# Performance work log

Hardware: AMD Instinct MI355X
Metric: run time of the kernel (lower is better)

Reference implementation:

```python
import jax, jax.numpy as jnp
import numpy as np

NUM_FEATURES = 256   # 2**8
BOND_DIM = 16
N_CORES = 8          # log2(NUM_FEATURES)
BATCH = 262144


def _mpo_cores(mpo_weights, n, bond_dim):
    # Slice the flat parameter vector into n cores of shape (l, r, 2, 2).
    shapes = [(1, bond_dim, 2, 2)] + [(bond_dim, bond_dim, 2, 2)] * (n - 2) + [(bond_dim, 1, 2, 2)]
    cores, off = [], 0
    for s in shapes:
        sz = int(np.prod(s))
        cores.append(mpo_weights[off:off + sz].reshape(s))
        off += sz
    return cores


def _contract_mpo(cores):
    # Sequentially contract the tensor-train cores into the full (2^n, 2^n) matrix.
    # T has axes (bond, I, J) where I/J accumulate the row/col physical bits
    # in order i1..in / j1..jn, matching the original einsum + reshape.
    T = cores[0][0]          # (r, 2, 2)
    dim = 2
    for A in cores[1:]:      # A: (l, r2, 2, 2)
        T = jnp.einsum('aIJ,abkm->bIkJm', T, A).reshape(A.shape[1], dim * 2, dim * 2)
        dim *= 2
    return T[0]              # (2^n, 2^n)


def setup_inputs() -> dict:
    key = jax.random.key(0)
    k1, k2, k3 = jax.random.split(key, 3)
    total = 2 * 4 * BOND_DIM + (N_CORES - 2) * 4 * BOND_DIM ** 2  # 6272
    return {
        'x': jax.random.normal(k1, (BATCH, NUM_FEATURES), dtype=jnp.float32),
        'mpo_weights': jax.random.normal(k2, (total,), dtype=jnp.float32) * 0.1,
        'dense_kernel': jax.random.normal(k3, (NUM_FEATURES, 1), dtype=jnp.float32) * 0.1,
        'dense_bias': jnp.zeros((1,), dtype=jnp.float32),
    }


def reference(x, mpo_weights, dense_kernel, dense_bias):
    W = _contract_mpo(_mpo_cores(mpo_weights, N_CORES, BOND_DIM))  # (256, 256)
    h = jnp.square(x @ W)                                          # (B, 256)
    return h @ dense_kernel + dense_bias                           # (B, 1)
```

## Files before the change

### kernel.cpp

```cpp
#include <hip/hip_runtime.h>
#include <hip/hip_bf16.h>

typedef _Float16 half8 __attribute__((ext_vector_type(8)));
typedef float    floatx4 __attribute__((ext_vector_type(4)));

#define WSCALE      4096.0f
#define WSCALE_INV  (1.0f/(4096.0f*4096.0f))

#define T1_OFF   0
#define U_OFF    4096
#define WF16_OFF 8192

__global__ __launch_bounds__(256)
void mpo_prep1(const float* __restrict__ w, float* __restrict__ ws) {
    __shared__ __align__(16) float wL[3136];
    __shared__ __align__(16) float sL[4352];
    const int tid = threadIdx.x;

    {
        const floatx4* s4 = reinterpret_cast<const floatx4*>(w + blockIdx.x * 3136);
        floatx4* d4 = reinterpret_cast<floatx4*>(wL);
        for (int i = tid; i < 784; i += 256) d4[i] = s4[i];
    }
    __syncthreads();

    if (blockIdx.x == 0) {
        {
            int li = tid;
            int mm = li & 3, kk = (li >> 2) & 3, c = li >> 4;
            int k1 = kk >> 1, k2 = kk & 1, m1 = mm >> 1, m2 = mm & 1;
            float s = 0.f;
#pragma unroll
            for (int b = 0; b < 16; ++b)
                s += wL[b * 4 + k1 * 2 + m1] * wL[64 + b * 64 + c * 4 + k2 * 2 + m2];
            sL[li] = s;
        }
        {
            const int i0 = (tid >> 4) * 4, j0 = (tid & 15) * 4;
            const float* Ab = wL + 1088 + (i0 >> 2) * 64;
            const float* Bb = wL + 2112 + j0;
            float acc[4][4] = {};
#pragma unroll
            for (int b = 0; b < 16; ++b) {
                floatx4 ar = *reinterpret_cast<const floatx4*>(Ab + b * 4);
                floatx4 br = *reinterpret_cast<const floatx4*>(Bb + b * 64);
#pragma unroll
                for (int r = 0; r < 4; ++r)
#pragma unroll
                    for (int s = 0; s < 4; ++s) acc[r][s] += ar[r] * br[s];
            }
#pragma unroll
            for (int r = 0; r < 4; ++r)
#pragma unroll
            for (int s = 0; s < 4; ++s) {
                int i = i0 + r, j = j0 + s;
                sL[256 + (i >> 2) * 256 + (j >> 2) * 16 +
                   ((i >> 1) & 1) * 8 + ((j >> 1) & 1) * 4 + (i & 1) * 2 + (j & 1)] = acc[r][s];
            }
        }
        __syncthreads();
        {
            const int p0 = (tid >> 6) * 4, q0 = (tid & 63) * 4;
            float acc[4][4] = {};
#pragma unroll
            for (int a = 0; a < 16; ++a) {
                floatx4 pr = *reinterpret_cast<const floatx4*>(sL + a * 16 + p0);
                floatx4 qr = *reinterpret_cast<const floatx4*>(sL + 256 + a * 256 + q0);
#pragma unroll
                for (int r = 0; r < 4; ++r)
#pragma unroll
                    for (int s = 0; s < 4; ++s) acc[r][s] += pr[r] * qr[s];
            }
#pragma unroll
            for (int r = 0; r < 4; ++r)
#pragma unroll
            for (int s = 0; s < 4; ++s) {
                int p = p0 + r, q = q0 + s;
                ws[T1_OFF + (q >> 4) * 256 + ((p >> 2) * 4 + ((q >> 2) & 3)) * 16 +
                   (p & 3) * 4 + (q & 3)] = acc[r][s];
            }
        }
    } else {
        {
            const int i0 = (tid >> 4) * 4, j0 = (tid & 15) * 4;
            const float* Ab = wL + (i0 >> 2) * 64;
            const float* Bb = wL + 1024 + j0;
            float acc[4][4] = {};
#pragma unroll
            for (int b = 0; b < 16; ++b) {
                floatx4 ar = *reinterpret_cast<const floatx4*>(Ab + b * 4);
                floatx4 br = *reinterpret_cast<const floatx4*>(Bb + b * 64);
#pragma unroll
                for (int r = 0; r < 4; ++r)
#pragma unroll
                    for (int s = 0; s < 4; ++s) acc[r][s] += ar[r] * br[s];
            }
#pragma unroll
            for (int r = 0; r < 4; ++r)
#pragma unroll
            for (int s = 0; s < 4; ++s) {
                int i = i0 + r, j = j0 + s;
                sL[(i >> 2) * 256 + (j >> 2) * 16 +
                   ((i >> 1) & 1) * 8 + ((j >> 1) & 1) * 4 + (i & 1) * 2 + (j & 1)] = acc[r][s];
            }
        }
        {
            int li = tid;
            int mm = li & 3, kk = (li >> 2) & 3, a = li >> 4;
            int k1 = kk >> 1, k2 = kk & 1, m1 = mm >> 1, m2 = mm & 1;
            float s = 0.f;
#pragma unroll
            for (int b = 0; b < 16; ++b)
                s += wL[2048 + a * 64 + b * 4 + k1 * 2 + m1] * wL[3072 + b * 4 + k2 * 2 + m2];
            sL[4096 + li] = s;
        }
        __syncthreads();
        {
            const int r0 = (tid >> 2) * 4, q0 = (tid & 3) * 4;
            float acc[4][4] = {};
#pragma unroll
            for (int b = 0; b < 16; ++b) {
                floatx4 ar = *reinterpret_cast<const floatx4*>(sL + (r0 >> 4) * 256 + b * 16 + (r0 & 15));
                floatx4 br = *reinterpret_cast<const floatx4*>(sL + 4096 + b * 16 + q0);
#pragma unroll
                for (int r = 0; r < 4; ++r)
#pragma unroll
                    for (int s = 0; s < 4; ++s) acc[r][s] += ar[r] * br[s];
            }
#pragma unroll
            for (int r = 0; r < 4; ++r)
#pragma unroll
            for (int s = 0; s < 4; ++s)
                ws[U_OFF + (r0 + r) * 16 + q0 + s] = acc[r][s];
        }
    }
}

__global__ __launch_bounds__(256)
void mpo_prep2(const float* __restrict__ ws, _Float16* __restrict__ Wf) {
    int idx = blockIdx.x * blockDim.x + threadIdx.x;
    int J4 = idx & 255, I4 = idx >> 8;
    int I16 = I4 >> 4, kc = (I4 >> 2) & 3, k2 = I4 & 3;
    int J16 = J4 >> 4, mc = (J4 >> 2) & 3, m2 = J4 & 3;
    const float* T1 = ws + T1_OFF;
    const float* U  = ws + U_OFF + (((kc * 4 + mc) * 4 + k2) * 4 + m2);
    float s = 0.f;
#pragma unroll
    for (int a = 0; a < 16; ++a)
        s += T1[(a * 16 + I16) * 16 + J16] * U[a * 256];
    int n = J4 >> 4, lr = J4 & 15, kk = I4 >> 5, gg = (I4 >> 3) & 3, j = I4 & 7;
    Wf[(((n * 8 + kk) * 64) + gg * 16 + lr) * 8 + j] = (_Float16)(s * WSCALE);
}

__global__ __launch_bounds__(512, 2)
void mpo_main(const float* __restrict__ x, const _Float16* __restrict__ Wf,
              const float* __restrict__ dk, const float* __restrict__ bias,
              float* __restrict__ out) {
    extern __shared__ _Float16 Wl[];
    float* dkL = reinterpret_cast<float*>(Wl + 65536);

    const int tid  = threadIdx.x;
    const int lane = tid & 63;
    const int wave = tid >> 6;
    const int lrow = lane & 15;
    const int g    = lane >> 4;

    const long blockbase = (long)blockIdx.x * 1024;
    const float* xb0 = x + (blockbase + wave * 16 + lrow) * 256 + g * 8;

    half8 a[8];
    floatx4 loE[8], hiE[8], loO[8], hiO[8];

#define SB()  __builtin_amdgcn_sched_barrier(0)
#define NTL(p) __builtin_nontemporal_load(reinterpret_cast<const floatx4*>(p))
#define XLDE(i, xn) do { const float* p_ = (xn) + (i) * 32; loE[i] = NTL(p_); hiE[i] = NTL(p_ + 4); } while (0)
#define XLDO(i, xn) do { const float* p_ = (xn) + (i) * 32; loO[i] = NTL(p_); hiO[i] = NTL(p_ + 4); } while (0)
#define XLDE_ALL(xn) do { XLDE(0,xn); XLDE(1,xn); XLDE(2,xn); XLDE(3,xn); \
                          XLDE(4,xn); XLDE(5,xn); XLDE(6,xn); XLDE(7,xn); } while (0)
#define XLDO_ALL(xn) do { XLDO(0,xn); XLDO(1,xn); XLDO(2,xn); XLDO(3,xn); \
                          XLDO(4,xn); XLDO(5,xn); XLDO(6,xn); XLDO(7,xn); } while (0)
#define XCVTE(i) do { half8 f_;                                                \
                     f_[0] = (_Float16)loE[i][0]; f_[1] = (_Float16)loE[i][1]; \
                     f_[2] = (_Float16)loE[i][2]; f_[3] = (_Float16)loE[i][3]; \
                     f_[4] = (_Float16)hiE[i][0]; f_[5] = (_Float16)hiE[i][1]; \
                     f_[6] = (_Float16)hiE[i][2]; f_[7] = (_Float16)hiE[i][3]; \
                     a[i] = f_; } while (0)
#define XCVTO(i) do { half8 f_;                                                \
                     f_[0] = (_Float16)loO[i][0]; f_[1] = (_Float16)loO[i][1]; \
                     f_[2] = (_Float16)loO[i][2]; f_[3] = (_Float16)loO[i][3]; \
                     f_[4] = (_Float16)hiO[i][0]; f_[5] = (_Float16)hiO[i][1]; \
                     f_[6] = (_Float16)hiO[i][2]; f_[7] = (_Float16)hiO[i][3]; \
                     a[i] = f_; } while (0)
#define XCVTE_ALL() do { XCVTE(0); XCVTE(1); XCVTE(2); XCVTE(3); \
                         XCVTE(4); XCVTE(5); XCVTE(6); XCVTE(7); } while (0)
#define XCVTO_ALL() do { XCVTO(0); XCVTO(1); XCVTO(2); XCVTO(3); \
                         XCVTO(4); XCVTO(5); XCVTO(6); XCVTO(7); } while (0)

#define NLOOP(rp) do {                                                           \
    _Pragma("unroll 1")                                                          \
    for (int n = 0; n < 16; ++n) {                                               \
        const float kv = dkL[n * 16 + lrow];                                     \
        const half8* Wn = Wv + n * 512 + lane;                                   \
        floatx4 c0 = {0, 0, 0, 0};                                               \
        _Pragma("unroll")                                                        \
        for (int kk = 0; kk < 8; ++kk)                                           \
            c0 = __builtin_amdgcn_mfma_f32_16x16x32_f16(a[kk], Wn[kk * 64], c0, 0, 0, 0); \
        _Pragma("unroll")                                                        \
        for (int r = 0; r < 4; ++r) rp[r] += c0[r] * c0[r] * kv;                 \
    } } while (0)

#define REDUCE_STORE(rp, p) do {                                                 \
    _Pragma("unroll")                                                            \
    for (int r = 0; r < 4; ++r) {                                                \
        float v = rp[r];                                                         \
        v += __shfl_xor(v, 1); v += __shfl_xor(v, 2);                            \
        v += __shfl_xor(v, 4); v += __shfl_xor(v, 8);                            \
        rp[r] = v;                                                               \
    }                                                                            \
    if (lrow == 0) {                                                             \
        floatx4 o;                                                               \
        _Pragma("unroll")                                                        \
        for (int r = 0; r < 4; ++r) o[r] = rp[r] * WSCALE_INV + bs;              \
        *reinterpret_cast<floatx4*>(out + blockbase + (p) * 128 + wave * 16 + g * 4) = o; \
    } } while (0)

    XLDE_ALL(xb0);
    SB();
    {
        const floatx4* src = reinterpret_cast<const floatx4*>(Wf);
        floatx4* dst = reinterpret_cast<floatx4*>(Wl);
#pragma unroll
        for (int i = 0; i < 16; ++i)
            dst[tid + i * 512] = src[tid + i * 512];
    }
    if (tid < 256) dkL[tid] = dk[tid];
    const float bs = bias[0];
    __syncthreads();
    XLDO_ALL(xb0 + 128 * 256);
    SB();
    XCVTE_ALL();
    SB();

    const half8* Wv = reinterpret_cast<const half8*>(Wl);

#pragma unroll 1
    for (int pp = 0; pp < 8; pp += 2) {
        {
            float rp[4] = {0, 0, 0, 0};
            NLOOP(rp);
            if (pp + 2 < 8) { XLDE_ALL(xb0 + (pp + 2) * (128 * 256)); }
            SB();
            REDUCE_STORE(rp, pp);
            XCVTO_ALL();
            SB();
        }
        {
            float rp[4] = {0, 0, 0, 0};
            NLOOP(rp);
            if (pp + 3 < 8) { XLDO_ALL(xb0 + (pp + 3) * (128 * 256)); }
            SB();
            REDUCE_STORE(rp, pp + 1);
            if (pp + 2 < 8) { XCVTE_ALL(); }
            SB();
        }
    }
}

extern "C" void kernel_launch(void* const* d_in, const int* in_sizes, int n_in,
                              void* d_out, int out_size, void* d_ws, size_t ws_size,
                              hipStream_t stream) {
    const float* x    = (const float*)d_in[0];
    const float* w    = (const float*)d_in[1];
    const float* dk   = (const float*)d_in[2];
    const float* bias = (const float*)d_in[3];
    float* out = (float*)d_out;
    float* ws  = (float*)d_ws;

    _Float16* Wf16 = (_Float16*)(ws + WF16_OFF);

    static bool attr_set = false;
    if (!attr_set) {
        hipFuncSetAttribute((const void*)mpo_main,
                            hipFuncAttributeMaxDynamicSharedMemorySize, 132096);
        attr_set = true;
    }

    mpo_prep1<<<2, 256, 0, stream>>>(w, ws);
    mpo_prep2<<<256, 256, 0, stream>>>(ws, Wf16);

    mpo_main<<<256, 512, 132096, stream>>>(x, Wf16, dk, bias, out);
}
```

Measured before the change: 73.96 us.

## Keep W slices in registers per wave and stage x tiles through LDS

Each wave now holds two 16-column W slices in registers instead of reading all of W from LDS for every MFMA. The 128-row x tile is converted to fp16 and staged in LDS so every wave reads all rows, and partial dot products are reduced across waves through a small LDS buffer. LDS footprint drops from about 129KB to 68KB, which could allow more blocks per CU. The cost is two block-wide barriers per tile and the loss of the even/odd double buffering of x loads, which is replaced by a single prefetch buffer.

```diff
diff --git a/kernel.cpp b/kernel.cpp
--- a/kernel.cpp
+++ b/kernel.cpp
@@ -156,8 +156,9 @@
 void mpo_main(const float* __restrict__ x, const _Float16* __restrict__ Wf,
               const float* __restrict__ dk, const float* __restrict__ bias,
               float* __restrict__ out) {
-    extern __shared__ _Float16 Wl[];
-    float* dkL = reinterpret_cast<float*>(Wl + 65536);
+    extern __shared__ __align__(16) char smem[];
+    half8* xL = reinterpret_cast<half8*>(smem);
+    float* pL = reinterpret_cast<float*>(smem + 65536);
 
     const int tid  = threadIdx.x;
     const int lane = tid & 63;
@@ -169,100 +170,89 @@
     const float* xb0 = x + (blockbase + wave * 16 + lrow) * 256 + g * 8;
 
     half8 a[8];
-    floatx4 loE[8], hiE[8], loO[8], hiO[8];
+    floatx4 lo[8], hi[8];
 
 #define SB()  __builtin_amdgcn_sched_barrier(0)
 #define NTL(p) __builtin_nontemporal_load(reinterpret_cast<const floatx4*>(p))
-#define XLDE(i, xn) do { const float* p_ = (xn) + (i) * 32; loE[i] = NTL(p_); hiE[i] = NTL(p_ + 4); } while (0)
-#define XLDO(i, xn) do { const float* p_ = (xn) + (i) * 32; loO[i] = NTL(p_); hiO[i] = NTL(p_ + 4); } while (0)
-#define XLDE_ALL(xn) do { XLDE(0,xn); XLDE(1,xn); XLDE(2,xn); XLDE(3,xn); \
-                          XLDE(4,xn); XLDE(5,xn); XLDE(6,xn); XLDE(7,xn); } while (0)
-#define XLDO_ALL(xn) do { XLDO(0,xn); XLDO(1,xn); XLDO(2,xn); XLDO(3,xn); \
-                          XLDO(4,xn); XLDO(5,xn); XLDO(6,xn); XLDO(7,xn); } while (0)
-#define XCVTE(i) do { half8 f_;                                                \
-                     f_[0] = (_Float16)loE[i][0]; f_[1] = (_Float16)loE[i][1]; \
-                     f_[2] = (_Float16)loE[i][2]; f_[3] = (_Float16)loE[i][3]; \
-                     f_[4] = (_Float16)hiE[i][0]; f_[5] = (_Float16)hiE[i][1]; \
-                     f_[6] = (_Float16)hiE[i][2]; f_[7] = (_Float16)hiE[i][3]; \
+#define XLD(i, xn) do { const float* p_ = (xn) + (i) * 32; lo[i] = NTL(p_); hi[i] = NTL(p_ + 4); } while (0)
+#define XLD_ALL(xn) do { XLD(0,xn); XLD(1,xn); XLD(2,xn); XLD(3,xn); \
+                         XLD(4,xn); XLD(5,xn); XLD(6,xn); XLD(7,xn); } while (0)
+#define XCVT(i) do { half8 f_;                                                \
+                     f_[0] = (_Float16)lo[i][0]; f_[1] = (_Float16)lo[i][1];  \
+                     f_[2] = (_Float16)lo[i][2]; f_[3] = (_Float16)lo[i][3];  \
+                     f_[4] = (_Float16)hi[i][0]; f_[5] = (_Float16)hi[i][1];  \
+                     f_[6] = (_Float16)hi[i][2]; f_[7] = (_Float16)hi[i][3];  \
                      a[i] = f_; } while (0)
-#define XCVTO(i) do { half8 f_;                                                \
-                     f_[0] = (_Float16)loO[i][0]; f_[1] = (_Float16)loO[i][1]; \
-                     f_[2] = (_Float16)loO[i][2]; f_[3] = (_Float16)loO[i][3]; \
-                     f_[4] = (_Float16)hiO[i][0]; f_[5] = (_Float16)hiO[i][1]; \
-                     f_[6] = (_Float16)hiO[i][2]; f_[7] = (_Float16)hiO[i][3]; \
-                     a[i] = f_; } while (0)
-#define XCVTE_ALL() do { XCVTE(0); XCVTE(1); XCVTE(2); XCVTE(3); \
-                         XCVTE(4); XCVTE(5); XCVTE(6); XCVTE(7); } while (0)
-#define XCVTO_ALL() do { XCVTO(0); XCVTO(1); XCVTO(2); XCVTO(3); \
-                         XCVTO(4); XCVTO(5); XCVTO(6); XCVTO(7); } while (0)
-
-#define NLOOP(rp) do {                                                           \
-    _Pragma("unroll 1")                                                          \
-    for (int n = 0; n < 16; ++n) {                                               \
-        const float kv = dkL[n * 16 + lrow];                                     \
-        const half8* Wn = Wv + n * 512 + lane;                                   \
-        floatx4 c0 = {0, 0, 0, 0};                                               \
-        _Pragma("unroll")                                                        \
-        for (int kk = 0; kk < 8; ++kk)                                           \
-            c0 = __builtin_amdgcn_mfma_f32_16x16x32_f16(a[kk], Wn[kk * 64], c0, 0, 0, 0); \
-        _Pragma("unroll")                                                        \
-        for (int r = 0; r < 4; ++r) rp[r] += c0[r] * c0[r] * kv;                 \
-    } } while (0)
-
-#define REDUCE_STORE(rp, p) do {                                                 \
-    _Pragma("unroll")                                                            \
-    for (int r = 0; r < 4; ++r) {                                                \
-        float v = rp[r];                                                         \
-        v += __shfl_xor(v, 1); v += __shfl_xor(v, 2);                            \
-        v += __shfl_xor(v, 4); v += __shfl_xor(v, 8);                            \
-        rp[r] = v;                                                               \
-    }                                                                            \
-    if (lrow == 0) {                                                             \
-        floatx4 o;                                                               \
-        _Pragma("unroll")                                                        \
-        for (int r = 0; r < 4; ++r) o[r] = rp[r] * WSCALE_INV + bs;              \
-        *reinterpret_cast<floatx4*>(out + blockbase + (p) * 128 + wave * 16 + g * 4) = o; \
-    } } while (0)
-
-    XLDE_ALL(xb0);
+#define XCVT_ALL() do { XCVT(0); XCVT(1); XCVT(2); XCVT(3); \
+                        XCVT(4); XCVT(5); XCVT(6); XCVT(7); } while (0)
+#define XSTORE_ALL() do { _Pragma("unroll") \
+    for (int kk = 0; kk < 8; ++kk) xL[(wave * 8 + kk) * 64 + lane] = a[kk]; } while (0)
+
+    XLD_ALL(xb0);
     SB();
+    half8 Wr0[8], Wr1[8];
     {
-        const floatx4* src = reinterpret_cast<const floatx4*>(Wf);
-        floatx4* dst = reinterpret_cast<floatx4*>(Wl);
-#pragma unroll
-        for (int i = 0; i < 16; ++i)
-            dst[tid + i * 512] = src[tid + i * 512];
-    }
-    if (tid < 256) dkL[tid] = dk[tid];
-    const float bs = bias[0];
+        const half8* Wg = reinterpret_cast<const half8*>(Wf);
+#pragma unroll
+        for (int kk = 0; kk < 8; ++kk) {
+            Wr0[kk] = Wg[((wave * 2) * 8 + kk) * 64 + lane];
+            Wr1[kk] = Wg[((wave * 2 + 1) * 8 + kk) * 64 + lane];
+        }
+    }
+    const float kv0 = dk[wave * 32 + lrow];
+    const float kv1 = dk[wave * 32 + 16 + lrow];
+    const float bs  = bias[0];
+    XCVT_ALL();
+    XSTORE_ALL();
     __syncthreads();
-    XLDO_ALL(xb0 + 128 * 256);
-    SB();
-    XCVTE_ALL();
-    SB();
-
-    const half8* Wv = reinterpret_cast<const half8*>(Wl);
 
 #pragma unroll 1
-    for (int pp = 0; pp < 8; pp += 2) {
-        {
-            float rp[4] = {0, 0, 0, 0};
-            NLOOP(rp);
-            if (pp + 2 < 8) { XLDE_ALL(xb0 + (pp + 2) * (128 * 256)); }
-            SB();
-            REDUCE_STORE(rp, pp);
-            XCVTO_ALL();
-            SB();
-        }
-        {
-            float rp[4] = {0, 0, 0, 0};
-            NLOOP(rp);
-            if (pp + 3 < 8) { XLDO_ALL(xb0 + (pp + 3) * (128 * 256)); }
-            SB();
-            REDUCE_STORE(rp, pp + 1);
-            if (pp + 2 < 8) { XCVTE_ALL(); }
-            SB();
-        }
+    for (int p = 0; p < 8; ++p) {
+        if (p < 7) { XLD_ALL(xb0 + (p + 1) * (128 * 256)); }
+        SB();
+
+#pragma unroll 1
+        for (int t = 0; t < 8; ++t) {
+            half8 at[8];
+#pragma unroll
+            for (int kk = 0; kk < 8; ++kk) at[kk] = xL[(t * 8 + kk) * 64 + lane];
+            floatx4 c0 = {0, 0, 0, 0}, c1 = {0, 0, 0, 0};
+#pragma unroll
+            for (int kk = 0; kk < 8; ++kk) {
+                c0 = __builtin_amdgcn_mfma_f32_16x16x32_f16(at[kk], Wr0[kk], c0, 0, 0, 0);
+                c1 = __builtin_amdgcn_mfma_f32_16x16x32_f16(at[kk], Wr1[kk], c1, 0, 0, 0);
+            }
+            floatx4 rp;
+#pragma unroll
+            for (int r = 0; r < 4; ++r)
+                rp[r] = c0[r] * c0[r] * kv0 + c1[r] * c1[r] * kv1;
+#pragma unroll
+            for (int r = 0; r < 4; ++r) {
+                float v = rp[r];
+                v += __shfl_xor(v, 1);
+                v += __shfl_xor(v, 2);
+                v += __shfl_xor(v, 4);
+                v += __shfl_xor(v, 8);
+                rp[r] = v;
+            }
+            if (lrow == 0)
+                *reinterpret_cast<floatx4*>(pL + ((t * 4 + g) * 8 + wave) * 4) = rp;
+        }
+        __syncthreads();
+
+        if (tid < 128) {
+            float s = 0.f;
+#pragma unroll
+            for (int w2 = 0; w2 < 8; ++w2)
+                s += pL[((tid >> 2) * 8 + w2) * 4 + (tid & 3)];
+            out[blockbase + p * 128 + tid] = s * WSCALE_INV + bs;
+        }
+
+        if (p < 7) {
+            XCVT_ALL();
+            XSTORE_ALL();
+        }
+        __syncthreads();
     }
 }
 
@@ -281,12 +271,12 @@
     static bool attr_set = false;
     if (!attr_set) {
         hipFuncSetAttribute((const void*)mpo_main,
-                            hipFuncAttributeMaxDynamicSharedMemorySize, 132096);
+                            hipFuncAttributeMaxDynamicSharedMemorySize, 69632);
         attr_set = true;
     }
 
     mpo_prep1<<<2, 256, 0, stream>>>(w, ws);
     mpo_prep2<<<256, 256, 0, stream>>>(ws, Wf16);
 
-    mpo_main<<<256, 512, 132096, stream>>>(x, Wf16, dk, bias, out);
-}
+    mpo_main<<<256, 512, 69632, stream>>>(x, Wf16, dk, bias, out);
+}
```

Result: slower. 96.09 us (+29.9%).
